# Performance work log

Measured on AMD Instinct MI355X. Metric: run time of the kernel, lower is better.

Reference implementation:

```python
import jax, jax.numpy as jnp
import numpy as np

STATE_DIM = 5
HIDDEN = 32
B, S = 128, 4096
D_IN = STATE_DIM + 1 + 3  # [h_prev, temp_seq, direction]


def setup_inputs() -> dict:
    key = jax.random.key(0)
    ks = jax.random.split(key, 16)
    g = lambda k, shp: (jax.random.normal(k, shp, dtype=jnp.float32) * 0.1)
    z = lambda shp: jnp.zeros(shp, jnp.float32)
    inp = {}
    inp["h_prev"] = jax.random.normal(ks[0], (B, S, STATE_DIM), dtype=jnp.float32)
    inp["delta_x"] = jax.random.uniform(ks[1], (B, S, 6), dtype=jnp.float32)
    # internal layer 0 (input D_IN -> HIDDEN), layer 1 (HIDDEN -> HIDDEN)
    inp["Wa0"] = g(ks[2], (D_IN, HIDDEN)); inp["ba0"] = z((HIDDEN,))
    inp["Wb0"] = g(ks[3], (D_IN, HIDDEN)); inp["bb0"] = z((HIDDEN,))
    inp["Wa1"] = g(ks[4], (HIDDEN, HIDDEN)); inp["ba1"] = z((HIDDEN,))
    inp["Wb1"] = g(ks[5], (HIDDEN, HIDDEN)); inp["bb1"] = z((HIDDEN,))
    inp["W_alpha"] = g(ks[6], (HIDDEN, 1)); inp["b_alpha"] = z((1,))
    inp["W_beta"]  = g(ks[7], (HIDDEN, 1)); inp["b_beta"]  = z((1,))
    inp["W_gamma"] = g(ks[8], (HIDDEN, 1)); inp["b_gamma"] = z((1,))
    inp["W_c"] = g(ks[9], (HIDDEN, STATE_DIM)); inp["b_c"] = z((STATE_DIM,))
    inp["W_out"] = g(ks[10], (STATE_DIM, 1))  # no bias
    return inp


def reference(h_prev, delta_x, Wa0, ba0, Wb0, bb0, Wa1, ba1, Wb1, bb1,
              W_alpha, b_alpha, W_beta, b_beta, W_gamma, b_gamma,
              W_c, b_c, W_out):
    # delta_x: [delta_strain, delta_time, delta_temp, init_strain, init_time, init_temp]
    df = delta_x[..., :3]                       # (B, S, 3)
    init_temp = delta_x[:, 0:1, 5:6]            # (B, 1, 1) init temp at t=0
    temp_seq = jnp.cumsum(delta_x[..., 2:3], axis=1) + init_temp  # (B, S, 1)
    # normalized increment direction
    norm = jnp.maximum(jnp.sqrt(jnp.sum(df * df, axis=-1, keepdims=True)), 1e-7)
    direction = df / norm                       # (B, S, 3)
    l = jnp.concatenate([h_prev, temp_seq, direction], axis=-1)   # (B, S, 9)
    # two internal tanh*tanh gated dense layers
    l = jnp.tanh(l @ Wa0 + ba0) * jnp.tanh(l @ Wb0 + bb0)         # (B, S, 32)
    l = jnp.tanh(l @ Wa1 + ba1) * jnp.tanh(l @ Wb1 + bb1)         # (B, S, 32)
    # exp gates (non-negative rate params)
    alpha = jnp.exp(l @ W_alpha + b_alpha)      # (B, S, 1)
    beta  = jnp.exp(l @ W_beta  + b_beta)
    gamma = jnp.exp(l @ W_gamma + b_gamma)
    c_n = jnp.tanh(l @ W_c + b_c)               # (B, S, 5)
    # update gate from physical increments
    z = 1.0 - jnp.exp(-alpha * jnp.abs(df[..., 0:1])
                      - beta * df[..., 1:2]
                      - gamma * jnp.abs(df[..., 2:3]))
    h_n = (1.0 - z) * h_prev + z * c_n          # (B, S, 5)
    sigma_n = h_n @ W_out                       # (B, S, 1)
    return (h_n, sigma_n)
```

## Files before the change

### kernel.cpp

```cpp
#include <hip/hip_runtime.h>

#define B_DIMC   128
#define S_DIMC   4096
#define N_TOK    (B_DIMC * S_DIMC)
#define CHUNK    512
#define NWAVE    8
#define N_CHUNK  (N_TOK / CHUNK)
#define CPB      (S_DIMC / CHUNK)

typedef __attribute__((ext_vector_type(8))) short  short8;
typedef __attribute__((ext_vector_type(4))) float  floatx4;
typedef __attribute__((ext_vector_type(4))) int    intx4;

__device__ __forceinline__ int cvtpk(float a, float b) {
    int r;
    asm("v_cvt_pk_bf16_f32 %0, %1, %2" : "=v"(r) : "v"(a), "v"(b));
    return r;
}

__device__ __forceinline__ float fast_tanh(float x) {
    float e = __builtin_amdgcn_exp2f(2.885390082f * __builtin_amdgcn_fmed3f(x, -9.0f, 9.0f));
    return fmaf(-2.0f, __builtin_amdgcn_rcpf(e + 1.0f), 1.0f);
}
__device__ __forceinline__ float gate2(float a, float b) {
    const float c = 2.885390082f;
    float ea = __builtin_amdgcn_exp2f(c * __builtin_amdgcn_fmed3f(a, -9.0f, 9.0f));
    float eb = __builtin_amdgcn_exp2f(c * __builtin_amdgcn_fmed3f(b, -9.0f, 9.0f));
    float t  = fmaf(ea, eb, 1.0f);
    float u  = ea + eb;
    return (t - u) * __builtin_amdgcn_rcpf(t + u);
}

__device__ __forceinline__ float head_w(int n, int k,
                                        const float* Wal, const float* Wbe,
                                        const float* Wga, const float* Wc) {
    if (n == 0) return Wal[k];
    if (n == 1) return Wbe[k];
    if (n == 2) return Wga[k];
    if (n < 8)  return Wc[k * 5 + (n - 3)];
    return 0.0f;
}


union SMemU {
    struct {
        short W[4][32][40];
        short Wh[16][40];
        float Bias[16];
        float Wsum[NWAVE];
        float Wpre[NWAVE];
    } b;
    short A[NWAVE][64][40];
};

__global__ __launch_bounds__(512) void msc_kernel(
    const float* __restrict__ h_prev, const float* __restrict__ dx,
    const float* __restrict__ Wa0, const float* __restrict__ ba0,
    const float* __restrict__ Wb0, const float* __restrict__ bb0,
    const float* __restrict__ Wa1, const float* __restrict__ ba1,
    const float* __restrict__ Wb1, const float* __restrict__ bb1,
    const float* __restrict__ W_alpha, const float* __restrict__ b_alpha,
    const float* __restrict__ W_beta,  const float* __restrict__ b_beta,
    const float* __restrict__ W_gamma, const float* __restrict__ b_gamma,
    const float* __restrict__ W_c,     const float* __restrict__ b_c,
    const float* __restrict__ W_out,
    float* __restrict__ out)
{
    __shared__ __align__(16) SMemU sm;

    const int tid  = threadIdx.x;
    const int w    = tid >> 6;
    const int lane = tid & 63;
    const int n    = lane & 15;
    const int quad = lane >> 4;
    const int t    = blockIdx.x * CHUNK + tid;

    const float* hp = h_prev + (size_t)t * 5;
    const float* d  = dx     + (size_t)t * 6;
    const float hp0 = hp[0], hp1 = hp[1], hp2 = hp[2], hp3 = hp[3], hp4 = hp[4];
    const float df0 = d[0], df1 = d[1], df2 = d[2];

    const int batch = blockIdx.x >> 3;
    const int cib   = blockIdx.x & 7;
    const float* dxb = dx + (size_t)batch * S_DIMC * 6;
    const int nf4 = cib * 768;
    float ps = 0.0f;
    for (int j = tid; j < nf4; j += 512) {
        const float4 v = *(const float4*)(dxb + j * 4);
        const int r = j % 3;
        if (r == 0) ps += v.z;
        if (r == 2) ps += v.x;
    }
    ps += __shfl_xor(ps, 1, 64);
    ps += __shfl_xor(ps, 2, 64);
    ps += __shfl_xor(ps, 4, 64);
    ps += __shfl_xor(ps, 8, 64);
    ps += __shfl_xor(ps, 16, 64);
    ps += __shfl_xor(ps, 32, 64);
    if (lane == 0) sm.b.Wpre[w] = ps;

    float w5a[2], w5b[2], bA0[2], bB0[2], bA1[2], bB1[2];
    #pragma unroll
    for (int nt = 0; nt < 2; ++nt) {
        const int col = nt * 16 + n;
        w5a[nt] = Wa0[5 * 32 + col];  w5b[nt] = Wb0[5 * 32 + col];
        bA0[nt] = ba0[col];           bB0[nt] = bb0[col];
        bA1[nt] = ba1[col];           bB1[nt] = bb1[col];
    }

    float x = df2;
    #pragma unroll
    for (int off = 1; off < 64; off <<= 1) {
        float y = __shfl_up(x, off, 64);
        if (lane >= off) x += y;
    }
    if (lane == 63) sm.b.Wsum[w] = x;

    {
        const int col = tid >> 4, kd = tid & 15;
        #pragma unroll
        for (int m = 0; m < 2; ++m) {
            const float* Wsrc = (m == 0) ? Wa0 : Wb0;
            const int k0 = kd * 2, k1 = k0 + 1;
            const float v0 = (k0 < 9 && k0 != 5) ? Wsrc[k0 * 32 + col] : 0.0f;
            const float v1 = (k1 < 9 && k1 != 5) ? Wsrc[k1 * 32 + col] : 0.0f;
            ((int*)&sm.b.W[m][col][0])[kd] = cvtpk(v0, v1);
        }
        #pragma unroll
        for (int m = 2; m < 4; ++m) {
            const float* Wsrc = (m == 2) ? Wa1 : Wb1;
            ((int*)&sm.b.W[m][col][0])[kd] =
                cvtpk(Wsrc[kd * 32 + col], Wsrc[(kd + 16) * 32 + col]);
        }
    }
    if (tid < 256) {
        const int hn = tid >> 4, kd = tid & 15;
        ((int*)&sm.b.Wh[hn][0])[kd] =
            cvtpk(head_w(hn, kd,      W_alpha, W_beta, W_gamma, W_c),
                  head_w(hn, kd + 16, W_alpha, W_beta, W_gamma, W_c));
    }
    if (tid < 16) {
        sm.b.Bias[tid] = (tid == 0) ? b_alpha[0] : (tid == 1) ? b_beta[0]
                       : (tid == 2) ? b_gamma[0] : (tid < 8) ? b_c[tid - 3] : 0.0f;
    }

    __syncthreads();

    short8 Ba0f[2], Bb0f[2], Ba1f[2], Bb1f[2], Bhf;
    #pragma unroll
    for (int nt = 0; nt < 2; ++nt) {
        const int col = nt * 16 + n;
        Ba0f[nt] = *(const short8*)&sm.b.W[0][col][quad * 8];
        Bb0f[nt] = *(const short8*)&sm.b.W[1][col][quad * 8];
        Ba1f[nt] = *(const short8*)&sm.b.W[2][col][quad * 8];
        Bb1f[nt] = *(const short8*)&sm.b.W[3][col][quad * 8];
    }
    Bhf = *(const short8*)&sm.b.Wh[n][quad * 8];
    const float hbias = sm.b.Bias[n];

    float coff = dxb[5];
    #pragma unroll
    for (int ww = 0; ww < NWAVE; ++ww) coff += sm.b.Wpre[ww];
    float pre = coff;
    #pragma unroll
    for (int ww = 0; ww < NWAVE - 1; ++ww) if (w > ww) pre += sm.b.Wsum[ww];
    const float temp_t = pre + x;

    __syncthreads();

    const float nrm = fmaxf(sqrtf(df0*df0 + df1*df1 + df2*df2), 1e-7f);
    const float inv = __builtin_amdgcn_rcpf(nrm);
    {
        int* arow = (int*)&sm.A[w][lane][0];
        intx4 v0 = { cvtpk(hp0, hp1), cvtpk(hp2, hp3),
                     cvtpk(hp4, 0.0f), cvtpk(df0*inv, df1*inv) };
        intx4 v1 = { cvtpk(df2*inv, 0.0f), 0, 0, 0 };
        intx4 z4 = { 0, 0, 0, 0 };
        *(intx4*)&arow[0]  = v0;
        *(intx4*)&arow[4]  = v1;
        *(intx4*)&arow[8]  = z4;
        *(intx4*)&arow[12] = z4;
        *(float*)&arow[16] = temp_t;
    }

    #pragma unroll
    for (int mt = 0; mt < 4; ++mt) {
        const short8 Af = *(const short8*)&sm.A[w][mt * 16 + n][quad * 8];
        const int rb = mt * 16 + quad * 4;
        floatx4 tv;
        #pragma unroll
        for (int r = 0; r < 4; ++r)
            tv[r] = *(const float*)&sm.A[w][rb + r][32];
        floatx4 g0, g1;
        {
            floatx4 Ca, Cb;
            #pragma unroll
            for (int r = 0; r < 4; ++r) {
                Ca[r] = fmaf(tv[r], w5a[0], bA0[0]);
                Cb[r] = fmaf(tv[r], w5b[0], bB0[0]);
            }
            Ca = __builtin_amdgcn_mfma_f32_16x16x32_bf16(Af, Ba0f[0], Ca, 0, 0, 0);
            Cb = __builtin_amdgcn_mfma_f32_16x16x32_bf16(Af, Bb0f[0], Cb, 0, 0, 0);
            #pragma unroll
            for (int r = 0; r < 4; ++r) g0[r] = gate2(Ca[r], Cb[r]);
        }
        {
            floatx4 Ca, Cb;
            #pragma unroll
            for (int r = 0; r < 4; ++r) {
                Ca[r] = fmaf(tv[r], w5a[1], bA0[1]);
                Cb[r] = fmaf(tv[r], w5b[1], bB0[1]);
            }
            Ca = __builtin_amdgcn_mfma_f32_16x16x32_bf16(Af, Ba0f[1], Ca, 0, 0, 0);
            Cb = __builtin_amdgcn_mfma_f32_16x16x32_bf16(Af, Bb0f[1], Cb, 0, 0, 0);
            #pragma unroll
            for (int r = 0; r < 4; ++r) g1[r] = gate2(Ca[r], Cb[r]);
        }
        #pragma unroll
        for (int r = 0; r < 4; ++r)
            ((int*)&sm.A[w][rb + r][0])[n] = cvtpk(g0[r], g1[r]);
    }

    #pragma unroll
    for (int mt = 0; mt < 4; ++mt) {
        const short8 Af = *(const short8*)&sm.A[w][mt * 16 + n][quad * 8];
        const int rb = mt * 16 + quad * 4;
        floatx4 g0, g1;
        {
            floatx4 Ca = { bA1[0], bA1[0], bA1[0], bA1[0] };
            floatx4 Cb = { bB1[0], bB1[0], bB1[0], bB1[0] };
            Ca = __builtin_amdgcn_mfma_f32_16x16x32_bf16(Af, Ba1f[0], Ca, 0, 0, 0);
            Cb = __builtin_amdgcn_mfma_f32_16x16x32_bf16(Af, Bb1f[0], Cb, 0, 0, 0);
            #pragma unroll
            for (int r = 0; r < 4; ++r) g0[r] = gate2(Ca[r], Cb[r]);
        }
        {
            floatx4 Ca = { bA1[1], bA1[1], bA1[1], bA1[1] };
            floatx4 Cb = { bB1[1], bB1[1], bB1[1], bB1[1] };
            Ca = __builtin_amdgcn_mfma_f32_16x16x32_bf16(Af, Ba1f[1], Ca, 0, 0, 0);
            Cb = __builtin_amdgcn_mfma_f32_16x16x32_bf16(Af, Bb1f[1], Cb, 0, 0, 0);
            #pragma unroll
            for (int r = 0; r < 4; ++r) g1[r] = gate2(Ca[r], Cb[r]);
        }
        #pragma unroll
        for (int r = 0; r < 4; ++r)
            ((int*)&sm.A[w][rb + r][0])[n] = cvtpk(g0[r], g1[r]);
    }

    short8 Ah[4];
    #pragma unroll
    for (int mt = 0; mt < 4; ++mt)
        Ah[mt] = *(const short8*)&sm.A[w][mt * 16 + n][quad * 8];
    asm volatile("" ::: "memory");

    float* hc = (float*)&sm.A[w][0][0];
    #pragma unroll
    for (int mt = 0; mt < 4; ++mt) {
        floatx4 C = { hbias, hbias, hbias, hbias };
        C = __builtin_amdgcn_mfma_f32_16x16x32_bf16(Ah[mt], Bhf, C, 0, 0, 0);
        if (n < 8) {
            #pragma unroll
            for (int r = 0; r < 4; ++r)
                hc[(mt * 16 + quad * 4 + r) * 13 + n] = C[r];
        }
    }
    asm volatile("" ::: "memory");

    const floatx4 h0v = *(const floatx4*)&hc[lane * 13];
    const floatx4 h1v = *(const floatx4*)&hc[lane * 13 + 4];

    const float alpha = __expf(h0v[0]);
    const float beta  = __expf(h0v[1]);
    const float gamma = __expf(h0v[2]);
    const float z     = 1.0f - __expf(-(alpha * fabsf(df0) + beta * df1 + gamma * fabsf(df2)));
    const float omz   = 1.0f - z;

    const float c0 = fast_tanh(h0v[3]), c1 = fast_tanh(h1v[0]), c2 = fast_tanh(h1v[1]),
                c3 = fast_tanh(h1v[2]), c4 = fast_tanh(h1v[3]);

    const float hn0 = omz * hp0 + z * c0;
    const float hn1 = omz * hp1 + z * c1;
    const float hn2 = omz * hp2 + z * c2;
    const float hn3 = omz * hp3 + z * c3;
    const float hn4 = omz * hp4 + z * c4;

    float* out_h = out + (size_t)t * 5;
    out_h[0] = hn0; out_h[1] = hn1; out_h[2] = hn2; out_h[3] = hn3; out_h[4] = hn4;
    out[(size_t)N_TOK * 5 + t] =
        hn0 * W_out[0] + hn1 * W_out[1] + hn2 * W_out[2] + hn3 * W_out[3] + hn4 * W_out[4];
}

extern "C" void kernel_launch(void* const* d_in, const int* in_sizes, int n_in,
                              void* d_out, int out_size, void* d_ws, size_t ws_size,
                              hipStream_t stream) {
    const float* h_prev  = (const float*)d_in[0];
    const float* dx      = (const float*)d_in[1];
    const float* Wa0     = (const float*)d_in[2];
    const float* ba0     = (const float*)d_in[3];
    const float* Wb0     = (const float*)d_in[4];
    const float* bb0     = (const float*)d_in[5];
    const float* Wa1     = (const float*)d_in[6];
    const float* ba1     = (const float*)d_in[7];
    const float* Wb1     = (const float*)d_in[8];
    const float* bb1     = (const float*)d_in[9];
    const float* W_alpha = (const float*)d_in[10];
    const float* b_alpha = (const float*)d_in[11];
    const float* W_beta  = (const float*)d_in[12];
    const float* b_beta  = (const float*)d_in[13];
    const float* W_gamma = (const float*)d_in[14];
    const float* b_gamma = (const float*)d_in[15];
    const float* W_c     = (const float*)d_in[16];
    const float* b_c     = (const float*)d_in[17];
    const float* W_out   = (const float*)d_in[18];
    float* out = (float*)d_out;

    msc_kernel<<<N_CHUNK, CHUNK, 0, stream>>>(
        h_prev, dx,
        Wa0, ba0, Wb0, bb0, Wa1, ba1, Wb1, bb1,
        W_alpha, b_alpha, W_beta, b_beta, W_gamma, b_gamma,
        W_c, b_c, W_out, out);
}
```

Measured before the change: 137.2 us.

## Precompute per-chunk temperature sums in a separate kernel for the cumsum prefix

Each block used to re-read every earlier chunk of its batch row to build the cumsum prefix, which is quadratic redundant traffic (up to 7 chunks of dx per block). A new pre-pass kernel computes one delta-temp sum per chunk into a global array. The main kernel then reads up to 7 of those sums and reduces them with shuffles. This adds a second kernel launch and a read of all of dx in the pre-pass, in exchange for removing the redundant prefix reads.

```diff
diff --git a/kernel.cpp b/kernel.cpp
--- a/kernel.cpp
+++ b/kernel.cpp
@@ -11,6 +11,8 @@
 typedef __attribute__((ext_vector_type(8))) short  short8;
 typedef __attribute__((ext_vector_type(4))) float  floatx4;
 typedef __attribute__((ext_vector_type(4))) int    intx4;
+
+__device__ float g_chunksums[N_CHUNK];
 
 __device__ __forceinline__ int cvtpk(float a, float b) {
     int r;
@@ -41,6 +43,31 @@
     return 0.0f;
 }
 
+__global__ __launch_bounds__(512) void chunksum_kernel(const float* __restrict__ dx) {
+    const int lane = threadIdx.x & 63;
+    const int wid  = threadIdx.x >> 6;
+    __shared__ float wsum[NWAVE];
+    const float* base = dx + (size_t)blockIdx.x * (CHUNK * 6);
+    float s = 0.0f;
+    #pragma unroll
+    for (int j = threadIdx.x; j < 768; j += 512) {
+        const float4 v = *(const float4*)(base + j * 4);
+        const int r = j % 3;
+        if (r == 0) s += v.z;
+        if (r == 2) s += v.x;
+    }
+    #pragma unroll
+    for (int off = 32; off >= 1; off >>= 1) s += __shfl_down(s, off, 64);
+    if (lane == 0) wsum[wid] = s;
+    __syncthreads();
+    if (threadIdx.x == 0) {
+        float t = 0.0f;
+        #pragma unroll
+        for (int i = 0; i < NWAVE; ++i) t += wsum[i];
+        g_chunksums[blockIdx.x] = t;
+    }
+}
+
 
 union SMemU {
     struct {
@@ -48,7 +75,6 @@
         short Wh[16][40];
         float Bias[16];
         float Wsum[NWAVE];
-        float Wpre[NWAVE];
     } b;
     short A[NWAVE][64][40];
 };
@@ -82,22 +108,13 @@
 
     const int batch = blockIdx.x >> 3;
     const int cib   = blockIdx.x & 7;
-    const float* dxb = dx + (size_t)batch * S_DIMC * 6;
-    const int nf4 = cib * 768;
-    float ps = 0.0f;
-    for (int j = tid; j < nf4; j += 512) {
-        const float4 v = *(const float4*)(dxb + j * 4);
-        const int r = j % 3;
-        if (r == 0) ps += v.z;
-        if (r == 2) ps += v.x;
-    }
-    ps += __shfl_xor(ps, 1, 64);
-    ps += __shfl_xor(ps, 2, 64);
-    ps += __shfl_xor(ps, 4, 64);
-    ps += __shfl_xor(ps, 8, 64);
-    ps += __shfl_xor(ps, 16, 64);
-    ps += __shfl_xor(ps, 32, 64);
-    if (lane == 0) sm.b.Wpre[w] = ps;
+    float cs = (lane < cib) ? g_chunksums[batch * CPB + lane] : 0.0f;
+    cs += __shfl_xor(cs, 1, 64);
+    cs += __shfl_xor(cs, 2, 64);
+    cs += __shfl_xor(cs, 4, 64);
+    const float csum = __builtin_bit_cast(float,
+        __builtin_amdgcn_readfirstlane(__builtin_bit_cast(int, cs)));
+    const float coff = dx[(size_t)batch * S_DIMC * 6 + 5] + csum;
 
     float w5a[2], w5b[2], bA0[2], bB0[2], bA1[2], bB1[2];
     #pragma unroll
@@ -158,9 +175,6 @@
     Bhf = *(const short8*)&sm.b.Wh[n][quad * 8];
     const float hbias = sm.b.Bias[n];
 
-    float coff = dxb[5];
-    #pragma unroll
-    for (int ww = 0; ww < NWAVE; ++ww) coff += sm.b.Wpre[ww];
     float pre = coff;
     #pragma unroll
     for (int ww = 0; ww < NWAVE - 1; ++ww) if (w > ww) pre += sm.b.Wsum[ww];
@@ -314,6 +328,7 @@
     const float* W_out   = (const float*)d_in[18];
     float* out = (float*)d_out;
 
+    chunksum_kernel<<<N_CHUNK, CHUNK, 0, stream>>>(dx);
     msc_kernel<<<N_CHUNK, CHUNK, 0, stream>>>(
         h_prev, dx,
         Wa0, ba0, Wb0, bb0, Wa1, ba1, Wb1, bb1,
```

New measurement: 129.8 us. 1.06x faster.
